# Optimization experiments

Measured on AMD Instinct MI355X. Metric: run time of the kernel, lower is better.

Reference implementation:

```python
import jax, jax.numpy as jnp
import numpy as np

B, N, D, H = 8, 1024, 1024, 16
HEAD_DIM = D // H
SCALING = HEAD_DIM ** (-0.5)
NEG = -1000000000.0


def setup_inputs() -> dict:
    key = jax.random.key(0)
    ks = jax.random.split(key, 7)
    x = jax.random.normal(ks[0], (B, N, D), dtype=jnp.float32)
    # variable-length batch: lengths in [N//2, N], mask[b, i] = i < len_b
    lengths = jax.random.randint(ks[1], (B,), N // 2, N + 1)
    mask = jnp.arange(N)[None, :] < lengths[:, None]  # [B, N] bool
    s = D ** (-0.5)
    Wk = jax.random.normal(ks[2], (D, D), dtype=jnp.float32) * s
    Wq = jax.random.normal(ks[3], (D, D), dtype=jnp.float32) * s
    Wv = jax.random.normal(ks[4], (D, D), dtype=jnp.float32) * s
    Wo = jax.random.normal(ks[5], (D, D), dtype=jnp.float32) * s
    bo = jnp.zeros((D,), dtype=jnp.float32)
    return {"x": x, "mask": mask, "Wk": Wk, "Wq": Wq, "Wv": Wv, "Wo": Wo, "bo": bo}


def reference(x, mask, Wk, Wq, Wv, Wo, bo):
    # torch nn.Linear: y = x @ W.T
    keys = (x @ Wk.T).reshape(B, N, H, HEAD_DIM)
    queries = (x @ Wq.T).reshape(B, N, H, HEAD_DIM)
    values = (x @ Wv.T).reshape(B, N, H, HEAD_DIM)
    # NOTE: faithful to source: keys on i, queries on j, softmax over j
    scores = jnp.einsum('bihx,bjhx->bhij', keys, queries) * SCALING  # [B,H,N,N]
    pair_mask = mask[:, None, :] & mask[:, :, None]                  # [B,N,N]
    scores = scores + jnp.where(pair_mask, 0.0, NEG)[:, None, :, :]
    attn = jax.nn.softmax(scores, axis=-1)
    out = jnp.einsum('bhij,bjhx->bihx', attn, values)                # [B,N,H,hd]
    out = out.reshape(B, N, D)
    out = out @ Wo.T + bo
    # source does out_dense[mask] (ragged); static-shape equivalent: zero padding
    return out * mask[:, :, None].astype(out.dtype)
```

## Files before the change

### kernel.cpp

```cpp
#include <hip/hip_runtime.h>

typedef unsigned short u16;
typedef __attribute__((ext_vector_type(8))) short short8;
typedef __attribute__((ext_vector_type(4))) short short4v;
typedef __attribute__((ext_vector_type(4))) float f32x4;
typedef __attribute__((ext_vector_type(16))) float f32x16;

#define MFMA16(a, b, c) __builtin_amdgcn_mfma_f32_16x16x32_bf16(a, b, c, 0, 0, 0)
#define MFMA32(a, b, c) __builtin_amdgcn_mfma_f32_32x32x16_bf16(a, b, c, 0, 0, 0)

#define BB 8
#define NN 1024
#define DD 1024
#define HH 16
#define HD 64
#define MM (BB * NN)
#define SCLOG2 0.18033688011112042f

static __device__ __forceinline__ u16 f2bf(float f) {
  unsigned u = __float_as_uint(f);
  u += 0x7fffu + ((u >> 16) & 1u);
  return (u16)(u >> 16);
}

static __device__ __forceinline__ void gld16(const void* g, void* l) {
  __builtin_amdgcn_global_load_lds((const __attribute__((address_space(1))) void*)g,
                                   (__attribute__((address_space(3))) void*)l, 16, 0, 0);
}

static __device__ __forceinline__ unsigned cvtpk(float lo, float hi) {
  unsigned r;
  asm("v_cvt_pk_bf16_f32 %0, %1, %2" : "=v"(r) : "v"(lo), "v"(hi));
  return r;
}

static __device__ __forceinline__ f32x16 zero16() {
  f32x16 v;
#pragma unroll
  for (int i = 0; i < 16; ++i) v[i] = 0.f;
  return v;
}

__global__ void lens_kernel(const unsigned char* __restrict__ mask, int* __restrict__ lens) {
  __shared__ int acc[BB];
  const int t = threadIdx.x;
  if (t < BB) acc[t] = 0;
  __syncthreads();
  const bool isbyte = (mask[1] != 0);
  for (int b = 0; b < BB; ++b) {
    int s = 0;
    if (isbyte) {
      for (int i = t; i < NN; i += 256) s += mask[(size_t)b * NN + i] ? 1 : 0;
    } else {
      const int* mi = (const int*)mask;
      for (int i = t; i < NN; i += 256) s += mi[(size_t)b * NN + i] != 0 ? 1 : 0;
    }
    if (s) atomicAdd(&acc[b], s);
  }
  __syncthreads();
  if (t < BB) lens[t] = acc[t];
}

__global__ __launch_bounds__(256) void cast_bf16_kernel(const float* __restrict__ in,
                                                        u16* __restrict__ out, int n8) {
  const int i = blockIdx.x * 256 + threadIdx.x;
  if (i >= n8) return;
  const f32x4* p = (const f32x4*)in + (size_t)i * 2;
  const f32x4 a = p[0], b = p[1];
  short8 o;
  o[0] = (short)f2bf(a[0]); o[1] = (short)f2bf(a[1]);
  o[2] = (short)f2bf(a[2]); o[3] = (short)f2bf(a[3]);
  o[4] = (short)f2bf(b[0]); o[5] = (short)f2bf(b[1]);
  o[6] = (short)f2bf(b[2]); o[7] = (short)f2bf(b[3]);
  *(short8*)(out + (size_t)i * 8) = o;
}

__global__ __launch_bounds__(256) void cast4_bf16_kernel(const float* __restrict__ a, const float* __restrict__ b,
                                                         const float* __restrict__ c, const float* __restrict__ d,
                                                         u16* __restrict__ oa, u16* __restrict__ ob,
                                                         u16* __restrict__ oc, u16* __restrict__ od) {
  const int i = blockIdx.x * 256 + threadIdx.x;
  const float* in;
  u16* out;
  switch (blockIdx.y) {
    case 0: in = a; out = oa; break;
    case 1: in = b; out = ob; break;
    case 2: in = c; out = oc; break;
    default: in = d; out = od; break;
  }
  const f32x4* p = (const f32x4*)in + (size_t)i * 2;
  const f32x4 va = p[0], vb = p[1];
  short8 o;
  o[0] = (short)f2bf(va[0]); o[1] = (short)f2bf(va[1]);
  o[2] = (short)f2bf(va[2]); o[3] = (short)f2bf(va[3]);
  o[4] = (short)f2bf(vb[0]); o[5] = (short)f2bf(vb[1]);
  o[6] = (short)f2bf(vb[2]); o[7] = (short)f2bf(vb[3]);
  *(short8*)(out + (size_t)i * 8) = o;
}

__global__ __launch_bounds__(256) void gemm_qkv(const u16* __restrict__ A,
                                                const u16* __restrict__ Wk3, const u16* __restrict__ Wq3,
                                                const u16* __restrict__ Wv3,
                                                u16* __restrict__ kb, u16* __restrict__ qb,
                                                u16* __restrict__ vtb) {
  constexpr int K = 1024;
  __shared__ u16 As[128 * 32];
  __shared__ u16 Bs[128 * 32];
  const int m0 = blockIdx.x * 128;
  const int mat = blockIdx.y >> 3;
  const int n0 = (blockIdx.y & 7) * 128;
  const u16* Bw = (mat == 0) ? Wk3 : (mat == 1) ? Wq3 : Wv3;
  const int t = threadIdx.x;
  const int lane = t & 63;
  const int w = t >> 6;
  const int wr = w >> 1, wc = w & 1;
  const int li = lane & 15, lg = lane >> 4;
  f32x4 acc[4][4] = {};
  const int off0 = t * 16, off1 = (256 + t) * 16;
  const int r0 = off0 >> 6, kb0 = (off0 & 63) >> 1;
  const int r1 = off1 >> 6, kb1 = (off1 & 63) >> 1;

  for (int k0 = 0; k0 < K; k0 += 32) {
    __syncthreads();
    gld16(A + (size_t)(m0 + r0) * K + k0 + kb0, As + off0 / 2);
    gld16(A + (size_t)(m0 + r1) * K + k0 + kb1, As + off1 / 2);
    gld16(Bw + (size_t)(n0 + r0) * K + k0 + kb0, Bs + off0 / 2);
    gld16(Bw + (size_t)(n0 + r1) * K + k0 + kb1, Bs + off1 / 2);
    __syncthreads();
    short8 af[4], bf[4];
#pragma unroll
    for (int mi = 0; mi < 4; ++mi)
      af[mi] = *(const short8*)(As + (wr * 64 + mi * 16 + li) * 32 + lg * 8);
#pragma unroll
    for (int ni = 0; ni < 4; ++ni)
      bf[ni] = *(const short8*)(Bs + (wc * 64 + ni * 16 + li) * 32 + lg * 8);
#pragma unroll
    for (int mi = 0; mi < 4; ++mi)
#pragma unroll
      for (int ni = 0; ni < 4; ++ni) acc[mi][ni] = MFMA16(af[mi], bf[ni], acc[mi][ni]);
  }

  if (mat == 2) {
#pragma unroll
    for (int mi = 0; mi < 4; ++mi) {
      const int row = m0 + wr * 64 + mi * 16 + lg * 4;
      const int bb = row >> 10, jj = row & 1023;
#pragma unroll
      for (int ni = 0; ni < 4; ++ni) {
        const int col = n0 + wc * 64 + ni * 16 + li;
        const int h = col >> 6, x = col & 63;
        short4v st;
#pragma unroll
        for (int r = 0; r < 4; ++r) st[r] = (short)f2bf(acc[mi][ni][r]);
        *(short4v*)(vtb + ((size_t)((bb * HH + h) * HD + x)) * NN + jj) = st;
      }
    }
  } else {
    u16* C = (mat == 0) ? kb : qb;
    const float scale = (mat == 0) ? SCLOG2 : 1.0f;
#pragma unroll
    for (int mi = 0; mi < 4; ++mi)
#pragma unroll
      for (int ni = 0; ni < 4; ++ni) {
        const int col = n0 + wc * 64 + ni * 16 + li;
        const int rowb = m0 + wr * 64 + mi * 16 + lg * 4;
#pragma unroll
        for (int r = 0; r < 4; ++r)
          C[(size_t)(rowb + r) * 1024 + col] = f2bf(acc[mi][ni][r] * scale);
      }
  }
}

__global__ __launch_bounds__(256) void gemm_out(const u16* __restrict__ A, const u16* __restrict__ Bw,
                                                float* __restrict__ C, const float* __restrict__ bias,
                                                const int* __restrict__ lens) {
  constexpr int K = 1024;
  __shared__ u16 As[128 * 32];
  __shared__ u16 Bs[128 * 32];
  const int m0 = blockIdx.x * 128;
  const int n0 = blockIdx.y * 128;
  const int t = threadIdx.x;
  const int lane = t & 63;
  const int w = t >> 6;
  const int wr = w >> 1, wc = w & 1;
  const int li = lane & 15, lg = lane >> 4;
  f32x4 acc[4][4] = {};
  const int off0 = t * 16, off1 = (256 + t) * 16;
  const int r0 = off0 >> 6, kb0 = (off0 & 63) >> 1;
  const int r1 = off1 >> 6, kb1 = (off1 & 63) >> 1;

  for (int k0 = 0; k0 < K; k0 += 32) {
    __syncthreads();
    gld16(A + (size_t)(m0 + r0) * K + k0 + kb0, As + off0 / 2);
    gld16(A + (size_t)(m0 + r1) * K + k0 + kb1, As + off1 / 2);
    gld16(Bw + (size_t)(n0 + r0) * K + k0 + kb0, Bs + off0 / 2);
    gld16(Bw + (size_t)(n0 + r1) * K + k0 + kb1, Bs + off1 / 2);
    __syncthreads();
    short8 af[4], bf[4];
#pragma unroll
    for (int mi = 0; mi < 4; ++mi)
      af[mi] = *(const short8*)(As + (wr * 64 + mi * 16 + li) * 32 + lg * 8);
#pragma unroll
    for (int ni = 0; ni < 4; ++ni)
      bf[ni] = *(const short8*)(Bs + (wc * 64 + ni * 16 + li) * 32 + lg * 8);
#pragma unroll
    for (int mi = 0; mi < 4; ++mi)
#pragma unroll
      for (int ni = 0; ni < 4; ++ni) acc[mi][ni] = MFMA16(af[mi], bf[ni], acc[mi][ni]);
  }

#pragma unroll
  for (int ni = 0; ni < 4; ++ni) {
    const int col = n0 + wc * 64 + ni * 16 + li;
    const float bv = bias[col];
#pragma unroll
    for (int mi = 0; mi < 4; ++mi) {
      const int rowb = m0 + wr * 64 + mi * 16 + lg * 4;
#pragma unroll
      for (int r = 0; r < 4; ++r) {
        const int row = rowb + r;
        const int bb = row >> 10, ii = row & 1023;
        const float v = (ii < lens[bb]) ? (acc[mi][ni][r] + bv) : 0.f;
        C[(size_t)row * 1024 + col] = v;
      }
    }
  }
}

__global__ __launch_bounds__(256) void attn_kernel(const u16* __restrict__ Kb, const u16* __restrict__ Qb,
                                                   const u16* __restrict__ Vtb, u16* __restrict__ attb,
                                                   const int* __restrict__ lens) {
  const int bid = blockIdx.x;
  const int work = (bid & 7) * 128 + (bid >> 3);
  const int ic = work & 7, h = (work >> 3) & 15, b = work >> 7;
  const int len = lens[b];
  const int i0 = ic * 128;
  if (i0 >= len) return;
  const int t = threadIdx.x;
  const int w = t >> 6, l = t & 63;
  const int l31 = l & 31, hi = l >> 5;
  const int i0w = i0 + w * 32;

  __shared__ u16 Qs[2][4096];
  __shared__ u16 Vs[2][4096];

  short8 kf[4];
  {
    const u16* kp = Kb + ((size_t)(b * NN + i0w + l31)) * DD + h * HD + hi * 8;
#pragma unroll
    for (int ks = 0; ks < 4; ++ks) kf[ks] = *(const short8*)(kp + ks * 16);
  }

  const size_t qsrc = ((size_t)(b * NN) + l31) * DD + h * HD + w * 16 + hi * 8;
  const size_t vsrc = ((size_t)((b * HH + h) * HD + l31)) * NN + w * 16 + hi * 8;

  auto STAGE = [&](int buf, int j0) {
    u16* qd = &Qs[buf][0] + t * 8;
    u16* vd = &Vs[buf][0] + t * 8;
    gld16(Qb + qsrc + (size_t)j0 * DD, qd);
    gld16(Qb + qsrc + (size_t)(j0 + 32) * DD, qd + 2048);
    gld16(Vtb + vsrc + j0, vd);
    gld16(Vtb + vsrc + 32 * NN + j0, vd + 2048);
  };

  f32x16 o0 = zero16(), o1 = zero16();
  float m_run = -3.0e38f, l_run = 0.f;
  const int nt = (len + 63) >> 6;

  STAGE(0, 0);
  __syncthreads();
  for (int jt = 0; jt < nt; ++jt) {
    const int cur = jt & 1;
    const int j0 = jt * 64;
    if (jt + 1 < nt) STAGE(cur ^ 1, j0 + 64);

    const u16* Qc = &Qs[cur][0];
    const u16* Vc = &Vs[cur][0];
    f32x16 s0 = zero16(), s1 = zero16();
    __builtin_amdgcn_s_setprio(1);
#pragma unroll
    for (int ks = 0; ks < 4; ++ks) {
      const short8 qf = *(const short8*)(Qc + (ks * 64 + l) * 8);
      s0 = MFMA32(qf, kf[ks], s0);
    }
#pragma unroll
    for (int ks = 0; ks < 4; ++ks) {
      const short8 qf = *(const short8*)(Qc + ((4 + ks) * 64 + l) * 8);
      s1 = MFMA32(qf, kf[ks], s1);
    }
    __builtin_amdgcn_s_setprio(0);

    if (j0 + 64 > len) {
#pragma unroll
      for (int r = 0; r < 16; ++r) {
        const int jl = (r & 3) + 8 * (r >> 2) + 4 * hi;
        if (j0 + jl >= len) s0[r] = -3.0e38f;
        if (j0 + 32 + jl >= len) s1[r] = -3.0e38f;
      }
    }

    float pmax = s0[0];
#pragma unroll
    for (int r = 1; r < 16; ++r) pmax = fmaxf(pmax, s0[r]);
#pragma unroll
    for (int r = 0; r < 16; ++r) pmax = fmaxf(pmax, s1[r]);
    pmax = fmaxf(pmax, __shfl_xor(pmax, 32));

    if (!__all(pmax <= m_run + 11.5f)) {
      const float mnew = fmaxf(m_run, pmax);
      const float al = __builtin_amdgcn_exp2f(m_run - mnew);
      l_run *= al;
#pragma unroll
      for (int r = 0; r < 16; ++r) { o0[r] *= al; o1[r] *= al; }
      m_run = mnew;
    }

    float rs = 0.f;
#pragma unroll
    for (int r = 0; r < 16; ++r) { const float p = __builtin_amdgcn_exp2f(s0[r] - m_run); s0[r] = p; rs += p; }
#pragma unroll
    for (int r = 0; r < 16; ++r) { const float p = __builtin_amdgcn_exp2f(s1[r] - m_run); s1[r] = p; rs += p; }
    rs += __shfl_xor(rs, 32);
    l_run += rs;

    short8 pf[4];
#pragma unroll
    for (int jk = 0; jk < 4; ++jk) {
      const f32x16& ss = (jk < 2) ? s0 : s1;
      const int kk = jk & 1;
      unsigned W0 = cvtpk(ss[8 * kk + 0], ss[8 * kk + 1]);
      unsigned W1 = cvtpk(ss[8 * kk + 2], ss[8 * kk + 3]);
      unsigned W2 = cvtpk(ss[8 * kk + 4], ss[8 * kk + 5]);
      unsigned W3 = cvtpk(ss[8 * kk + 6], ss[8 * kk + 7]);
      asm("v_permlane32_swap_b32 %0, %1" : "+v"(W0), "+v"(W2));
      asm("v_permlane32_swap_b32 %0, %1" : "+v"(W1), "+v"(W3));
      union { unsigned u[4]; short8 s; } pu;
      pu.u[0] = W0; pu.u[1] = W1; pu.u[2] = W2; pu.u[3] = W3;
      pf[jk] = pu.s;
    }

    __builtin_amdgcn_s_setprio(1);
#pragma unroll
    for (int kkg = 0; kkg < 4; ++kkg) {
      const short8 vf = *(const short8*)(Vc + (kkg * 64 + l) * 8);
      o0 = MFMA32(vf, pf[kkg], o0);
    }
#pragma unroll
    for (int kkg = 0; kkg < 4; ++kkg) {
      const short8 vf = *(const short8*)(Vc + ((4 + kkg) * 64 + l) * 8);
      o1 = MFMA32(vf, pf[kkg], o1);
    }
    __builtin_amdgcn_s_setprio(0);
    __syncthreads();
  }

  const float inv = 1.f / l_run;
  u16* op = attb + (size_t)(b * NN + i0w + l31) * DD + h * HD + hi * 4;
#pragma unroll
  for (int xs = 0; xs < 2; ++xs) {
    const f32x16& oo = xs ? o1 : o0;
#pragma unroll
    for (int q = 0; q < 4; ++q) {
      short4v st;
#pragma unroll
      for (int e = 0; e < 4; ++e) st[e] = (short)f2bf(oo[q * 4 + e] * inv);
      *(short4v*)(op + xs * 32 + q * 8) = st;
    }
  }
}

extern "C" void kernel_launch(void* const* d_in, const int* in_sizes, int n_in,
                              void* d_out, int out_size, void* d_ws, size_t ws_size,
                              hipStream_t stream) {
  const float* x = (const float*)d_in[0];
  const unsigned char* mask = (const unsigned char*)d_in[1];
  const float* Wk = (const float*)d_in[2];
  const float* Wq = (const float*)d_in[3];
  const float* Wv = (const float*)d_in[4];
  const float* Wo = (const float*)d_in[5];
  const float* bo = (const float*)d_in[6];
  float* out = (float*)d_out;

  char* ws = (char*)d_ws;
  size_t o = 0;
  int* lens = (int*)(ws + o); o += 256;
  u16* xb  = (u16*)(ws + o); o += (size_t)MM * DD * 2;
  u16* wkb = (u16*)(ws + o); o += (size_t)DD * DD * 2;
  u16* wqb = (u16*)(ws + o); o += (size_t)DD * DD * 2;
  u16* wvb = (u16*)(ws + o); o += (size_t)DD * DD * 2;
  u16* wob = (u16*)(ws + o); o += (size_t)DD * DD * 2;
  u16* kb  = (u16*)(ws + o); o += (size_t)MM * DD * 2;
  u16* qb  = (u16*)(ws + o); o += (size_t)MM * DD * 2;
  u16* vtb = (u16*)(ws + o); o += (size_t)MM * DD * 2;
  u16* attb = xb;

  lens_kernel<<<dim3(1), dim3(256), 0, stream>>>(mask, lens);

  const int xn8 = MM * DD / 8;
  cast_bf16_kernel<<<dim3(xn8 / 256), dim3(256), 0, stream>>>(x, xb, xn8);
  cast4_bf16_kernel<<<dim3(DD * DD / 8 / 256, 4), dim3(256), 0, stream>>>(
      Wk, Wq, Wv, Wo, wkb, wqb, wvb, wob);

  gemm_qkv<<<dim3(MM / 128, 24), dim3(256), 0, stream>>>(xb, wkb, wqb, wvb, kb, qb, vtb);

  attn_kernel<<<dim3(1024), dim3(256), 0, stream>>>(kb, qb, vtb, attb, lens);

  gemm_out<<<dim3(MM / 128, DD / 128), dim3(256), 0, stream>>>(attb, wob, out, bo, lens);
}
```

Before: 200.3 us.

## Skip padded row tiles in GEMMs, widen K-tile with swizzle, drop attention LDS staging

Both GEMMs now skip 128-row tiles that lie entirely past the sequence length; the output GEMM writes zeros for those tiles instead of computing them. The GEMM K-step doubles to 64 with an XOR-swizzled shared-memory layout and raised MFMA priority, cutting syncs per K and avoiding bank conflicts. The attention kernel drops its double-buffered LDS staging of Q and V and loads the fragments straight from global memory into registers, removing block-level barriers. The risk is that the direct global loads are less coalesced and raise register pressure.

```diff
diff --git a/kernel.cpp b/kernel.cpp
--- a/kernel.cpp
+++ b/kernel.cpp
@@ -98,15 +98,46 @@
   *(short8*)(out + (size_t)i * 8) = o;
 }
 
+#define GEMM_CORE(A_, B_)                                                       \
+  for (int k0 = 0; k0 < 1024; k0 += 64) {                                       \
+    __syncthreads();                                                            \
+    _Pragma("unroll") for (int p = 0; p < 4; ++p) {                             \
+      const int off = (p * 256 + t) * 16;                                       \
+      const int row = off >> 7;                                                 \
+      const int colb = (off & 127) ^ ((row & 7) << 4);                          \
+      gld16(A_ + (size_t)(m0 + row) * 1024 + k0 + (colb >> 1), As + off / 2);   \
+      gld16(B_ + (size_t)(n0 + row) * 1024 + k0 + (colb >> 1), Bs + off / 2);   \
+    }                                                                           \
+    __syncthreads();                                                            \
+    _Pragma("unroll") for (int ks = 0; ks < 2; ++ks) {                          \
+      short8 af[4], bf[4];                                                      \
+      _Pragma("unroll") for (int mi = 0; mi < 4; ++mi) {                        \
+        const int row = wr * 64 + mi * 16 + li;                                 \
+        const int byo = row * 128 + ((ks * 64 + lg * 16) ^ ((row & 7) << 4));   \
+        af[mi] = *(const short8*)((const char*)As + byo);                       \
+      }                                                                         \
+      _Pragma("unroll") for (int ni = 0; ni < 4; ++ni) {                        \
+        const int row = wc * 64 + ni * 16 + li;                                 \
+        const int byo = row * 128 + ((ks * 64 + lg * 16) ^ ((row & 7) << 4));   \
+        bf[ni] = *(const short8*)((const char*)Bs + byo);                       \
+      }                                                                         \
+      __builtin_amdgcn_s_setprio(1);                                            \
+      _Pragma("unroll") for (int mi = 0; mi < 4; ++mi)                          \
+        _Pragma("unroll") for (int ni = 0; ni < 4; ++ni)                        \
+            acc[mi][ni] = MFMA16(af[mi], bf[ni], acc[mi][ni]);                  \
+      __builtin_amdgcn_s_setprio(0);                                            \
+    }                                                                           \
+  }
+
 __global__ __launch_bounds__(256) void gemm_qkv(const u16* __restrict__ A,
                                                 const u16* __restrict__ Wk3, const u16* __restrict__ Wq3,
                                                 const u16* __restrict__ Wv3,
                                                 u16* __restrict__ kb, u16* __restrict__ qb,
-                                                u16* __restrict__ vtb) {
-  constexpr int K = 1024;
-  __shared__ u16 As[128 * 32];
-  __shared__ u16 Bs[128 * 32];
+                                                u16* __restrict__ vtb, const int* __restrict__ lens) {
   const int m0 = blockIdx.x * 128;
+  if ((m0 & 1023) >= lens[m0 >> 10]) return;
+  __shared__ u16 As[128 * 64];
+  __shared__ u16 Bs[128 * 64];
   const int mat = blockIdx.y >> 3;
   const int n0 = (blockIdx.y & 7) * 128;
   const u16* Bw = (mat == 0) ? Wk3 : (mat == 1) ? Wq3 : Wv3;
@@ -116,29 +147,8 @@
   const int wr = w >> 1, wc = w & 1;
   const int li = lane & 15, lg = lane >> 4;
   f32x4 acc[4][4] = {};
-  const int off0 = t * 16, off1 = (256 + t) * 16;
-  const int r0 = off0 >> 6, kb0 = (off0 & 63) >> 1;
-  const int r1 = off1 >> 6, kb1 = (off1 & 63) >> 1;
-
-  for (int k0 = 0; k0 < K; k0 += 32) {
-    __syncthreads();
-    gld16(A + (size_t)(m0 + r0) * K + k0 + kb0, As + off0 / 2);
-    gld16(A + (size_t)(m0 + r1) * K + k0 + kb1, As + off1 / 2);
-    gld16(Bw + (size_t)(n0 + r0) * K + k0 + kb0, Bs + off0 / 2);
-    gld16(Bw + (size_t)(n0 + r1) * K + k0 + kb1, Bs + off1 / 2);
-    __syncthreads();
-    short8 af[4], bf[4];
-#pragma unroll
-    for (int mi = 0; mi < 4; ++mi)
-      af[mi] = *(const short8*)(As + (wr * 64 + mi * 16 + li) * 32 + lg * 8);
-#pragma unroll
-    for (int ni = 0; ni < 4; ++ni)
-      bf[ni] = *(const short8*)(Bs + (wc * 64 + ni * 16 + li) * 32 + lg * 8);
-#pragma unroll
-    for (int mi = 0; mi < 4; ++mi)
-#pragma unroll
-      for (int ni = 0; ni < 4; ++ni) acc[mi][ni] = MFMA16(af[mi], bf[ni], acc[mi][ni]);
-  }
+
+  GEMM_CORE(A, Bw)
 
   if (mat == 2) {
 #pragma unroll
@@ -174,40 +184,26 @@
 __global__ __launch_bounds__(256) void gemm_out(const u16* __restrict__ A, const u16* __restrict__ Bw,
                                                 float* __restrict__ C, const float* __restrict__ bias,
                                                 const int* __restrict__ lens) {
-  constexpr int K = 1024;
-  __shared__ u16 As[128 * 32];
-  __shared__ u16 Bs[128 * 32];
   const int m0 = blockIdx.x * 128;
   const int n0 = blockIdx.y * 128;
   const int t = threadIdx.x;
+  if ((m0 & 1023) >= lens[m0 >> 10]) {
+    const int r = t >> 1, ch = (t & 1) * 64;
+    float* Crow = C + (size_t)(m0 + r) * 1024 + n0 + ch;
+    const f32x4 z = {0.f, 0.f, 0.f, 0.f};
+#pragma unroll
+    for (int c = 0; c < 16; ++c) *(f32x4*)(Crow + c * 4) = z;
+    return;
+  }
+  __shared__ u16 As[128 * 64];
+  __shared__ u16 Bs[128 * 64];
   const int lane = t & 63;
   const int w = t >> 6;
   const int wr = w >> 1, wc = w & 1;
   const int li = lane & 15, lg = lane >> 4;
   f32x4 acc[4][4] = {};
-  const int off0 = t * 16, off1 = (256 + t) * 16;
-  const int r0 = off0 >> 6, kb0 = (off0 & 63) >> 1;
-  const int r1 = off1 >> 6, kb1 = (off1 & 63) >> 1;
-
-  for (int k0 = 0; k0 < K; k0 += 32) {
-    __syncthreads();
-    gld16(A + (size_t)(m0 + r0) * K + k0 + kb0, As + off0 / 2);
-    gld16(A + (size_t)(m0 + r1) * K + k0 + kb1, As + off1 / 2);
-    gld16(Bw + (size_t)(n0 + r0) * K + k0 + kb0, Bs + off0 / 2);
-    gld16(Bw + (size_t)(n0 + r1) * K + k0 + kb1, Bs + off1 / 2);
-    __syncthreads();
-    short8 af[4], bf[4];
-#pragma unroll
-    for (int mi = 0; mi < 4; ++mi)
-      af[mi] = *(const short8*)(As + (wr * 64 + mi * 16 + li) * 32 + lg * 8);
-#pragma unroll
-    for (int ni = 0; ni < 4; ++ni)
-      bf[ni] = *(const short8*)(Bs + (wc * 64 + ni * 16 + li) * 32 + lg * 8);
-#pragma unroll
-    for (int mi = 0; mi < 4; ++mi)
-#pragma unroll
-      for (int ni = 0; ni < 4; ++ni) acc[mi][ni] = MFMA16(af[mi], bf[ni], acc[mi][ni]);
-  }
+
+  GEMM_CORE(A, Bw)
 
 #pragma unroll
   for (int ni = 0; ni < 4; ++ni) {
@@ -241,54 +237,41 @@
   const int l31 = l & 31, hi = l >> 5;
   const int i0w = i0 + w * 32;
 
-  __shared__ u16 Qs[2][4096];
-  __shared__ u16 Vs[2][4096];
-
   short8 kf[4];
   {
     const u16* kp = Kb + ((size_t)(b * NN + i0w + l31)) * DD + h * HD + hi * 8;
 #pragma unroll
     for (int ks = 0; ks < 4; ++ks) kf[ks] = *(const short8*)(kp + ks * 16);
   }
-
-  const size_t qsrc = ((size_t)(b * NN) + l31) * DD + h * HD + w * 16 + hi * 8;
-  const size_t vsrc = ((size_t)((b * HH + h) * HD + l31)) * NN + w * 16 + hi * 8;
-
-  auto STAGE = [&](int buf, int j0) {
-    u16* qd = &Qs[buf][0] + t * 8;
-    u16* vd = &Vs[buf][0] + t * 8;
-    gld16(Qb + qsrc + (size_t)j0 * DD, qd);
-    gld16(Qb + qsrc + (size_t)(j0 + 32) * DD, qd + 2048);
-    gld16(Vtb + vsrc + j0, vd);
-    gld16(Vtb + vsrc + 32 * NN + j0, vd + 2048);
-  };
+  const u16* qp = Qb + ((size_t)(b * NN) + l31) * DD + h * HD + hi * 8;
+  const u16* vp = Vtb + ((size_t)((b * HH + h) * HD) + l31) * NN + hi * 8;
 
   f32x16 o0 = zero16(), o1 = zero16();
   float m_run = -3.0e38f, l_run = 0.f;
   const int nt = (len + 63) >> 6;
 
-  STAGE(0, 0);
-  __syncthreads();
   for (int jt = 0; jt < nt; ++jt) {
-    const int cur = jt & 1;
     const int j0 = jt * 64;
-    if (jt + 1 < nt) STAGE(cur ^ 1, j0 + 64);
-
-    const u16* Qc = &Qs[cur][0];
-    const u16* Vc = &Vs[cur][0];
+    short8 qf0[4], qf1[4];
+#pragma unroll
+    for (int ks = 0; ks < 4; ++ks) {
+      qf0[ks] = *(const short8*)(qp + (size_t)j0 * DD + ks * 16);
+      qf1[ks] = *(const short8*)(qp + (size_t)(j0 + 32) * DD + ks * 16);
+    }
     f32x16 s0 = zero16(), s1 = zero16();
     __builtin_amdgcn_s_setprio(1);
 #pragma unroll
-    for (int ks = 0; ks < 4; ++ks) {
-      const short8 qf = *(const short8*)(Qc + (ks * 64 + l) * 8);
-      s0 = MFMA32(qf, kf[ks], s0);
-    }
-#pragma unroll
-    for (int ks = 0; ks < 4; ++ks) {
-      const short8 qf = *(const short8*)(Qc + ((4 + ks) * 64 + l) * 8);
-      s1 = MFMA32(qf, kf[ks], s1);
-    }
+    for (int ks = 0; ks < 4; ++ks) s0 = MFMA32(qf0[ks], kf[ks], s0);
+#pragma unroll
+    for (int ks = 0; ks < 4; ++ks) s1 = MFMA32(qf1[ks], kf[ks], s1);
     __builtin_amdgcn_s_setprio(0);
+
+    short8 vf0[4], vf1[4];
+#pragma unroll
+    for (int kk = 0; kk < 4; ++kk) {
+      vf0[kk] = *(const short8*)(vp + j0 + kk * 16);
+      vf1[kk] = *(const short8*)(vp + (size_t)32 * NN + j0 + kk * 16);
+    }
 
     if (j0 + 64 > len) {
 #pragma unroll
@@ -342,16 +325,10 @@
     __builtin_amdgcn_s_setprio(1);
 #pragma unroll
     for (int kkg = 0; kkg < 4; ++kkg) {
-      const short8 vf = *(const short8*)(Vc + (kkg * 64 + l) * 8);
-      o0 = MFMA32(vf, pf[kkg], o0);
-    }
-#pragma unroll
-    for (int kkg = 0; kkg < 4; ++kkg) {
-      const short8 vf = *(const short8*)(Vc + ((4 + kkg) * 64 + l) * 8);
-      o1 = MFMA32(vf, pf[kkg], o1);
+      o0 = MFMA32(vf0[kkg], pf[kkg], o0);
+      o1 = MFMA32(vf1[kkg], pf[kkg], o1);
     }
     __builtin_amdgcn_s_setprio(0);
-    __syncthreads();
   }
 
   const float inv = 1.f / l_run;
@@ -401,7 +378,7 @@
   cast4_bf16_kernel<<<dim3(DD * DD / 8 / 256, 4), dim3(256), 0, stream>>>(
       Wk, Wq, Wv, Wo, wkb, wqb, wvb, wob);
 
-  gemm_qkv<<<dim3(MM / 128, 24), dim3(256), 0, stream>>>(xb, wkb, wqb, wvb, kb, qb, vtb);
+  gemm_qkv<<<dim3(MM / 128, 24), dim3(256), 0, stream>>>(xb, wkb, wqb, wvb, kb, qb, vtb, lens);
 
   attn_kernel<<<dim3(1024), dim3(256), 0, stream>>>(kb, qb, vtb, attb, lens);
 
```

After: 235.8 us. 17.8% more time.
